# Optimization experiments

Measured on AMD Instinct MI355X. Metric: run time of the kernel, lower is better.

## Reference

```python
import jax, jax.numpy as jnp
import numpy as np

B, S, D, V = 256, 128, 768, 30522
MASK_ID = 103
# vocab ids of the label words (8 positive, 6 neutral, 7 negative)
LABEL_IDS = [
    [2307, 2204, 3835, 2157, 6581, 2986, 5151, 3893],
    [7929, 24791, 8699, 4257, 16021, 6623],
    [6659, 2919, 11771, 3532, 11325, 4997, 13135],
]


def setup_inputs() -> dict:
    key = jax.random.key(0)
    ks = jax.random.split(key, 12)
    length = jax.random.randint(ks[0], (B,), 5, 105)          # 3+length <= 108 < S
    input_ids = jax.random.randint(ks[1], (B, S), 200, 30000)  # never hits MASK_ID
    input_ids = input_ids.at[jnp.arange(B), 3 + length].set(MASK_ID)  # one [MASK] per row
    bert_out = jax.random.normal(ks[2], (B, S, D), dtype=jnp.float32)
    p = lambda k, shp: 0.02 * jax.random.normal(k, shp, dtype=jnp.float32)
    return {
        'bert_out': bert_out,
        'input_ids': input_ids,
        'length': length,
        'senti_w': p(ks[3], (2, D)), 'senti_b': p(ks[4], (2,)),
        'dense_w': p(ks[5], (D, 2 * D)), 'dense_b': p(ks[6], (D,)),
        'dec_w': p(ks[7], (V, D)), 'dec_b': p(ks[8], (V,)),
        'w0': p(ks[9], (2, 8)), 'w1': p(ks[10], (2, 6)), 'w2': p(ks[11], (2, 7)),
    }


def reference(bert_out, input_ids, length, senti_w, senti_b, dense_w, dense_b,
              dec_w, dec_b, w0, w1, w2):
    # pooler -> sentiment head (Dropout is identity at inference)
    pooler = bert_out[:, 0]                                   # [B, D]
    category_out = pooler @ senti_w.T + senti_b               # [B, 2]

    # per-row [MASK] hidden state (exactly one MASK_ID per row)
    mask_pos = jnp.argmax(input_ids == MASK_ID, axis=1)       # [B]
    mask_logits = jnp.take_along_axis(bert_out, mask_pos[:, None, None], axis=1)[:, 0]  # [B, D]

    # attention(): softmax over the ragged slice bert_out[i, 3:3+length[i]]
    scores_raw = jnp.einsum('bsd,bd->bs', bert_out, mask_logits)        # [B, S]
    idx = jnp.arange(S)
    valid = (idx[None, :] >= 3) & (idx[None, :] < 3 + length[:, None])  # [B, S]
    scores = jax.nn.softmax(jnp.where(valid, scores_raw, -jnp.inf), axis=1)
    scores = jnp.where(valid, scores, 0.0)
    att = jnp.einsum('bs,bsd->bd', scores, bert_out)          # [B, D]

    feats = jnp.concatenate([att, mask_logits], axis=1)       # [B, 2D]
    h = jnp.tanh(feats @ dense_w.T + dense_b)                 # [B, D]
    probs = jnp.tanh(h @ dec_w.T + dec_b)                     # [B, V]

    outs = []
    for ids, w in zip(LABEL_IDS, (w0, w1, w2)):
        lp = probs[:, jnp.array(ids)]                         # [B, k]
        outs.append(lp @ w.T)                                 # [B, 2]
    out = jnp.stack(outs, axis=2)                             # [B, 2, 3]
    return category_out, out
```

## Files before the change

### kernel.cpp

```cpp
#include <hip/hip_runtime.h>
#include <hip/hip_bf16.h>
#include <math.h>

#define BB 256
#define SS 128
#define DD 768
#define K2 1536
#define MASK_ID 103

typedef __attribute__((ext_vector_type(8))) short short8;
typedef __attribute__((ext_vector_type(4))) float floatx4;

__constant__ int c_ids[21] = {
    2307, 2204, 3835, 2157, 6581, 2986, 5151, 3893,
    7929, 24791, 8699, 4257, 16021, 6623,
    6659, 2919, 11771, 3532, 11325, 4997, 13135
};

__device__ __forceinline__ float waveReduceSum(float v) {
    #pragma unroll
    for (int off = 32; off > 0; off >>= 1) v += __shfl_down(v, off, 64);
    return v;
}
__device__ __forceinline__ float waveReduceSumAll(float v) {
    #pragma unroll
    for (int off = 32; off > 0; off >>= 1) v += __shfl_xor(v, off, 64);
    return v;
}
__device__ __forceinline__ unsigned short f2bf(float f) {
    unsigned int u = __float_as_uint(f);
    u += 0x7FFF + ((u >> 16) & 1);
    return (unsigned short)(u >> 16);
}

__global__ __launch_bounds__(256) void k_cvt(
    const float* __restrict__ src, unsigned short* __restrict__ dst, int n4)
{
    int i = blockIdx.x * 256 + threadIdx.x;
    if (i < n4) {
        float4 v = ((const float4*)src)[i];
        ushort4 o;
        o.x = f2bf(v.x); o.y = f2bf(v.y); o.z = f2bf(v.z); o.w = f2bf(v.w);
        ((ushort4*)dst)[i] = o;
    }
}

__global__ __launch_bounds__(1024) void k_att(
    const float* __restrict__ bert, const int* __restrict__ ids,
    const int* __restrict__ len, const float* __restrict__ senti_w,
    const float* __restrict__ senti_b, float* __restrict__ cat_out,
    unsigned short* __restrict__ feats)
{
    __shared__ __align__(16) float s_mask[DD];
    __shared__ __align__(16) float s_part[16][DD];
    __shared__ float s_m[16], s_l[16], s_scale[16];
    __shared__ float s_red[32];
    __shared__ float s_M;
    __shared__ int s_mp;

    const int b = blockIdx.x;
    const int tid = threadIdx.x;
    const int lane = tid & 63;
    const int wave = tid >> 6;

    if (tid == 0) s_mp = SS;
    __syncthreads();
    if (tid < SS && ids[b * SS + tid] == MASK_ID) atomicMin(&s_mp, tid);
    __syncthreads();
    const int mp = (s_mp == SS) ? 0 : s_mp;
    const int L = len[b];
    const float* base = bert + (size_t)b * SS * DD;
    const float* mrow = base + (size_t)mp * DD;

    float c0 = 0.f, c1 = 0.f;
    if (tid < DD) {
        s_mask[tid] = mrow[tid];
        float x = base[tid];
        c0 = x * senti_w[tid];
        c1 = x * senti_w[DD + tid];
    }
    c0 = waveReduceSum(c0);
    c1 = waveReduceSum(c1);
    if (lane == 0) { s_red[wave] = c0; s_red[16 + wave] = c1; }
    __syncthreads();
    if (tid == 0) {
        float t0 = 0.f, t1 = 0.f;
        #pragma unroll
        for (int w = 0; w < 16; ++w) { t0 += s_red[w]; t1 += s_red[16 + w]; }
        cat_out[b * 2 + 0] = t0 + senti_b[0];
        cat_out[b * 2 + 1] = t1 + senti_b[1];
    }

    const float4* m4 = (const float4*)s_mask;
    float4 mm0 = m4[lane], mm1 = m4[lane + 64], mm2 = m4[lane + 128];
    float4 A0 = {0,0,0,0}, A1 = {0,0,0,0}, A2 = {0,0,0,0};
    float mloc = -INFINITY, lloc = 0.f;
    for (int s = 3 + wave; s < 3 + L; s += 16) {
        const float4* row = (const float4*)(base + (size_t)s * DD);
        float4 r0 = row[lane], r1 = row[lane + 64], r2 = row[lane + 128];
        float d = r0.x * mm0.x + r0.y * mm0.y + r0.z * mm0.z + r0.w * mm0.w
                + r1.x * mm1.x + r1.y * mm1.y + r1.z * mm1.z + r1.w * mm1.w
                + r2.x * mm2.x + r2.y * mm2.y + r2.z * mm2.z + r2.w * mm2.w;
        d = waveReduceSumAll(d);
        float mnew = fmaxf(mloc, d);
        float scale = __expf(mloc - mnew);
        float p = __expf(d - mnew);
        lloc = lloc * scale + p;
        A0.x = A0.x * scale + p * r0.x; A0.y = A0.y * scale + p * r0.y;
        A0.z = A0.z * scale + p * r0.z; A0.w = A0.w * scale + p * r0.w;
        A1.x = A1.x * scale + p * r1.x; A1.y = A1.y * scale + p * r1.y;
        A1.z = A1.z * scale + p * r1.z; A1.w = A1.w * scale + p * r1.w;
        A2.x = A2.x * scale + p * r2.x; A2.y = A2.y * scale + p * r2.y;
        A2.z = A2.z * scale + p * r2.z; A2.w = A2.w * scale + p * r2.w;
        mloc = mnew;
    }
    if (lane == 0) { s_m[wave] = mloc; s_l[wave] = lloc; }
    float4* pw = (float4*)s_part[wave];
    pw[lane] = A0; pw[lane + 64] = A1; pw[lane + 128] = A2;
    __syncthreads();

    if (tid == 0) {
        float M = -INFINITY;
        #pragma unroll
        for (int w = 0; w < 16; ++w) M = fmaxf(M, s_m[w]);
        s_M = M;
    }
    __syncthreads();
    if (tid < 16) s_scale[tid] = __expf(s_m[tid] - s_M);
    __syncthreads();

    if (tid < DD) {
        float lt = 0.f, a = 0.f;
        #pragma unroll
        for (int w = 0; w < 16; ++w) {
            lt += s_scale[w] * s_l[w];
            a  += s_scale[w] * s_part[w][tid];
        }
        unsigned short* fb = feats + (size_t)b * K2;
        fb[tid]      = f2bf(a / lt);
        fb[DD + tid] = f2bf(s_mask[tid]);
    }
}

__global__ __launch_bounds__(256) void k_dense(
    const unsigned short* __restrict__ featsb,
    const unsigned short* __restrict__ dwb,
    const float* __restrict__ db, float* __restrict__ h)
{
    const int tid = threadIdx.x;
    const int lane = tid & 63, wave = tid >> 6;
    const int b0 = blockIdx.y * 32 + (wave >> 1) * 16;
    const int j0 = blockIdx.x * 32 + (wave & 1) * 16;
    const int m = lane & 15, q = lane >> 4;

    const short8* Arow = (const short8*)(featsb + (size_t)(b0 + m) * K2);
    const short8* Brow = (const short8*)(dwb + (size_t)(j0 + m) * K2);
    floatx4 acc = {0.f, 0.f, 0.f, 0.f};
    #pragma unroll 8
    for (int k8 = 0; k8 < K2 / 8; k8 += 4) {
        short8 a = Arow[k8 + q];
        short8 w = Brow[k8 + q];
        acc = __builtin_amdgcn_mfma_f32_16x16x32_bf16(a, w, acc, 0, 0, 0);
    }
    const int col = j0 + m;
    const int rb = b0 + q * 4;
    const float bias = db[col];
    #pragma unroll
    for (int r = 0; r < 4; ++r)
        h[(size_t)(rb + r) * DD + col] = tanhf(acc[r] + bias);
}

__global__ __launch_bounds__(256) void k_dec(
    const float* __restrict__ h, const float* __restrict__ dec_w,
    const float* __restrict__ dec_b, const float* __restrict__ w0,
    const float* __restrict__ w1, const float* __restrict__ w2,
    float* __restrict__ out)
{
    __shared__ __align__(16) float s_h[DD];
    __shared__ float s_p[21];
    const int b = blockIdx.x;
    const int tid = threadIdx.x;
    const int lane = tid & 63, wave = tid >> 6;

    for (int d = tid; d < DD; d += 256) s_h[d] = h[(size_t)b * DD + d];
    __syncthreads();

    for (int idx = wave; idx < 21; idx += 4) {
        const int vid = c_ids[idx];
        const float* wr = dec_w + (size_t)vid * DD;
        float acc = 0.f;
        #pragma unroll
        for (int i = 0; i < DD / 64; ++i)
            acc += s_h[lane + 64 * i] * wr[lane + 64 * i];
        acc = waveReduceSum(acc);
        if (lane == 0) s_p[idx] = tanhf(acc + dec_b[vid]);
    }
    __syncthreads();

    if (tid < 6) {
        const int c = tid / 3, g = tid % 3;
        const float* wg = (g == 0) ? w0 : (g == 1) ? w1 : w2;
        const int n    = (g == 0) ? 8  : (g == 1) ? 6  : 7;
        const int base = (g == 0) ? 0  : (g == 1) ? 8  : 14;
        float acc = 0.f;
        for (int i = 0; i < n; ++i) acc += s_p[base + i] * wg[c * n + i];
        out[(size_t)b * 6 + c * 3 + g] = acc;
    }
}

extern "C" void kernel_launch(void* const* d_in, const int* in_sizes, int n_in,
                              void* d_out, int out_size, void* d_ws, size_t ws_size,
                              hipStream_t stream) {
    const float* bert    = (const float*)d_in[0];
    const int*   ids     = (const int*)  d_in[1];
    const int*   len     = (const int*)  d_in[2];
    const float* senti_w = (const float*)d_in[3];
    const float* senti_b = (const float*)d_in[4];
    const float* dense_w = (const float*)d_in[5];
    const float* dense_b = (const float*)d_in[6];
    const float* dec_w   = (const float*)d_in[7];
    const float* dec_b   = (const float*)d_in[8];
    const float* w0      = (const float*)d_in[9];
    const float* w1      = (const float*)d_in[10];
    const float* w2      = (const float*)d_in[11];
    float* out = (float*)d_out;

    unsigned short* feats = (unsigned short*)d_ws;
    unsigned short* dwb   = feats + (size_t)BB * K2;
    float* h = (float*)(dwb + (size_t)DD * K2);

    const int n4 = DD * K2 / 4;
    k_cvt<<<(n4 + 255) / 256, 256, 0, stream>>>(dense_w, dwb, n4);
    k_att<<<BB, 1024, 0, stream>>>(bert, ids, len, senti_w, senti_b, out, feats);
    k_dense<<<dim3(24, 8), 256, 0, stream>>>(feats, dwb, dense_b, h);
    k_dec<<<BB, 256, 0, stream>>>(h, dec_w, dec_b, w0, w1, w2, out + BB * 2);
}
```

Measured before the change: 224.4 us.

## Fuse dense weight conversion into attention kernel, unroll rows, split-K dense GEMM

The separate fp32-to-bf16 conversion kernel for dense_w is removed and its work is spread across the attention kernel's blocks, saving one launch and overlapping the conversion with the attention reads. The online-softmax loop now processes two rows per wave per iteration to raise memory-level parallelism and halve the rescale steps. The dense MFMA kernel splits K across two wave groups with a shared-memory reduction, doubling the waves in flight for the small GEMM. The conversion adds memory traffic inside the attention kernel, and the split-K adds a block-level sync.

```diff
diff --git a/kernel.cpp b/kernel.cpp
--- a/kernel.cpp
+++ b/kernel.cpp
@@ -33,23 +33,12 @@
     return (unsigned short)(u >> 16);
 }
 
-__global__ __launch_bounds__(256) void k_cvt(
-    const float* __restrict__ src, unsigned short* __restrict__ dst, int n4)
-{
-    int i = blockIdx.x * 256 + threadIdx.x;
-    if (i < n4) {
-        float4 v = ((const float4*)src)[i];
-        ushort4 o;
-        o.x = f2bf(v.x); o.y = f2bf(v.y); o.z = f2bf(v.z); o.w = f2bf(v.w);
-        ((ushort4*)dst)[i] = o;
-    }
-}
-
 __global__ __launch_bounds__(1024) void k_att(
     const float* __restrict__ bert, const int* __restrict__ ids,
     const int* __restrict__ len, const float* __restrict__ senti_w,
     const float* __restrict__ senti_b, float* __restrict__ cat_out,
-    unsigned short* __restrict__ feats)
+    unsigned short* __restrict__ feats,
+    const float* __restrict__ dense_w, unsigned short* __restrict__ dwb)
 {
     __shared__ __align__(16) float s_mask[DD];
     __shared__ __align__(16) float s_part[16][DD];
@@ -64,6 +53,17 @@
     const int wave = tid >> 6;
 
     if (tid == 0) s_mp = SS;
+
+    {
+        const int n4 = DD * K2 / 4;
+        for (int i = b * 1024 + tid; i < n4; i += BB * 1024) {
+            float4 v = ((const float4*)dense_w)[i];
+            ushort4 o;
+            o.x = f2bf(v.x); o.y = f2bf(v.y); o.z = f2bf(v.z); o.w = f2bf(v.w);
+            ((ushort4*)dwb)[i] = o;
+        }
+    }
+
     __syncthreads();
     if (tid < SS && ids[b * SS + tid] == MASK_ID) atomicMin(&s_mp, tid);
     __syncthreads();
@@ -95,23 +95,50 @@
     float4 mm0 = m4[lane], mm1 = m4[lane + 64], mm2 = m4[lane + 128];
     float4 A0 = {0,0,0,0}, A1 = {0,0,0,0}, A2 = {0,0,0,0};
     float mloc = -INFINITY, lloc = 0.f;
-    for (int s = 3 + wave; s < 3 + L; s += 16) {
-        const float4* row = (const float4*)(base + (size_t)s * DD);
-        float4 r0 = row[lane], r1 = row[lane + 64], r2 = row[lane + 128];
-        float d = r0.x * mm0.x + r0.y * mm0.y + r0.z * mm0.z + r0.w * mm0.w
-                + r1.x * mm1.x + r1.y * mm1.y + r1.z * mm1.z + r1.w * mm1.w
-                + r2.x * mm2.x + r2.y * mm2.y + r2.z * mm2.z + r2.w * mm2.w;
-        d = waveReduceSumAll(d);
-        float mnew = fmaxf(mloc, d);
+    int s = 3 + wave;
+    for (; s + 16 < 3 + L; s += 32) {
+        const float4* ra = (const float4*)(base + (size_t)s * DD);
+        const float4* rb = (const float4*)(base + (size_t)(s + 16) * DD);
+        float4 a0 = ra[lane], a1 = ra[lane + 64], a2 = ra[lane + 128];
+        float4 b0 = rb[lane], b1 = rb[lane + 64], b2 = rb[lane + 128];
+        float d1 = a0.x*mm0.x + a0.y*mm0.y + a0.z*mm0.z + a0.w*mm0.w
+                 + a1.x*mm1.x + a1.y*mm1.y + a1.z*mm1.z + a1.w*mm1.w
+                 + a2.x*mm2.x + a2.y*mm2.y + a2.z*mm2.z + a2.w*mm2.w;
+        float d2 = b0.x*mm0.x + b0.y*mm0.y + b0.z*mm0.z + b0.w*mm0.w
+                 + b1.x*mm1.x + b1.y*mm1.y + b1.z*mm1.z + b1.w*mm1.w
+                 + b2.x*mm2.x + b2.y*mm2.y + b2.z*mm2.z + b2.w*mm2.w;
+        d1 = waveReduceSumAll(d1);
+        d2 = waveReduceSumAll(d2);
+        float mnew = fmaxf(mloc, fmaxf(d1, d2));
         float scale = __expf(mloc - mnew);
-        float p = __expf(d - mnew);
-        lloc = lloc * scale + p;
-        A0.x = A0.x * scale + p * r0.x; A0.y = A0.y * scale + p * r0.y;
-        A0.z = A0.z * scale + p * r0.z; A0.w = A0.w * scale + p * r0.w;
-        A1.x = A1.x * scale + p * r1.x; A1.y = A1.y * scale + p * r1.y;
-        A1.z = A1.z * scale + p * r1.z; A1.w = A1.w * scale + p * r1.w;
-        A2.x = A2.x * scale + p * r2.x; A2.y = A2.y * scale + p * r2.y;
-        A2.z = A2.z * scale + p * r2.z; A2.w = A2.w * scale + p * r2.w;
+        float p1 = __expf(d1 - mnew);
+        float p2 = __expf(d2 - mnew);
+        lloc = lloc * scale + p1 + p2;
+        A0.x = A0.x*scale + p1*a0.x + p2*b0.x; A0.y = A0.y*scale + p1*a0.y + p2*b0.y;
+        A0.z = A0.z*scale + p1*a0.z + p2*b0.z; A0.w = A0.w*scale + p1*a0.w + p2*b0.w;
+        A1.x = A1.x*scale + p1*a1.x + p2*b1.x; A1.y = A1.y*scale + p1*a1.y + p2*b1.y;
+        A1.z = A1.z*scale + p1*a1.z + p2*b1.z; A1.w = A1.w*scale + p1*a1.w + p2*b1.w;
+        A2.x = A2.x*scale + p1*a2.x + p2*b2.x; A2.y = A2.y*scale + p1*a2.y + p2*b2.y;
+        A2.z = A2.z*scale + p1*a2.z + p2*b2.z; A2.w = A2.w*scale + p1*a2.w + p2*b2.w;
+        mloc = mnew;
+    }
+    for (; s < 3 + L; s += 16) {
+        const float4* ra = (const float4*)(base + (size_t)s * DD);
+        float4 a0 = ra[lane], a1 = ra[lane + 64], a2 = ra[lane + 128];
+        float d1 = a0.x*mm0.x + a0.y*mm0.y + a0.z*mm0.z + a0.w*mm0.w
+                 + a1.x*mm1.x + a1.y*mm1.y + a1.z*mm1.z + a1.w*mm1.w
+                 + a2.x*mm2.x + a2.y*mm2.y + a2.z*mm2.z + a2.w*mm2.w;
+        d1 = waveReduceSumAll(d1);
+        float mnew = fmaxf(mloc, d1);
+        float scale = __expf(mloc - mnew);
+        float p1 = __expf(d1 - mnew);
+        lloc = lloc * scale + p1;
+        A0.x = A0.x*scale + p1*a0.x; A0.y = A0.y*scale + p1*a0.y;
+        A0.z = A0.z*scale + p1*a0.z; A0.w = A0.w*scale + p1*a0.w;
+        A1.x = A1.x*scale + p1*a1.x; A1.y = A1.y*scale + p1*a1.y;
+        A1.z = A1.z*scale + p1*a1.z; A1.w = A1.w*scale + p1*a1.w;
+        A2.x = A2.x*scale + p1*a2.x; A2.y = A2.y*scale + p1*a2.y;
+        A2.z = A2.z*scale + p1*a2.z; A2.w = A2.w*scale + p1*a2.w;
         mloc = mnew;
     }
     if (lane == 0) { s_m[wave] = mloc; s_l[wave] = lloc; }
@@ -142,32 +169,40 @@
     }
 }
 
-__global__ __launch_bounds__(256) void k_dense(
+__global__ __launch_bounds__(512) void k_dense(
     const unsigned short* __restrict__ featsb,
     const unsigned short* __restrict__ dwb,
     const float* __restrict__ db, float* __restrict__ h)
 {
+    __shared__ floatx4 s_acc[4][64];
     const int tid = threadIdx.x;
     const int lane = tid & 63, wave = tid >> 6;
-    const int b0 = blockIdx.y * 32 + (wave >> 1) * 16;
-    const int j0 = blockIdx.x * 32 + (wave & 1) * 16;
+    const int wq = wave & 3, kh = wave >> 2;
+    const int b0 = blockIdx.y * 32 + (wq >> 1) * 16;
+    const int j0 = blockIdx.x * 32 + (wq & 1) * 16;
     const int m = lane & 15, q = lane >> 4;
 
-    const short8* Arow = (const short8*)(featsb + (size_t)(b0 + m) * K2);
-    const short8* Brow = (const short8*)(dwb + (size_t)(j0 + m) * K2);
+    const short8* Arow = (const short8*)(featsb + (size_t)(b0 + m) * K2) + kh * 96;
+    const short8* Brow = (const short8*)(dwb + (size_t)(j0 + m) * K2) + kh * 96;
     floatx4 acc = {0.f, 0.f, 0.f, 0.f};
-    #pragma unroll 8
-    for (int k8 = 0; k8 < K2 / 8; k8 += 4) {
+    #pragma unroll 6
+    for (int k8 = 0; k8 < 96; k8 += 4) {
         short8 a = Arow[k8 + q];
         short8 w = Brow[k8 + q];
         acc = __builtin_amdgcn_mfma_f32_16x16x32_bf16(a, w, acc, 0, 0, 0);
     }
-    const int col = j0 + m;
-    const int rb = b0 + q * 4;
-    const float bias = db[col];
-    #pragma unroll
-    for (int r = 0; r < 4; ++r)
-        h[(size_t)(rb + r) * DD + col] = tanhf(acc[r] + bias);
+    if (kh) s_acc[wq][lane] = acc;
+    __syncthreads();
+    if (!kh) {
+        floatx4 o = s_acc[wq][lane];
+        acc.x += o.x; acc.y += o.y; acc.z += o.z; acc.w += o.w;
+        const int col = j0 + m;
+        const int rb = b0 + q * 4;
+        const float bias = db[col];
+        #pragma unroll
+        for (int r = 0; r < 4; ++r)
+            h[(size_t)(rb + r) * DD + col] = tanhf(acc[r] + bias);
+    }
 }
 
 __global__ __launch_bounds__(256) void k_dec(
@@ -229,9 +264,8 @@
     unsigned short* dwb   = feats + (size_t)BB * K2;
     float* h = (float*)(dwb + (size_t)DD * K2);
 
-    const int n4 = DD * K2 / 4;
-    k_cvt<<<(n4 + 255) / 256, 256, 0, stream>>>(dense_w, dwb, n4);
-    k_att<<<BB, 1024, 0, stream>>>(bert, ids, len, senti_w, senti_b, out, feats);
-    k_dense<<<dim3(24, 8), 256, 0, stream>>>(feats, dwb, dense_b, h);
+    k_att<<<BB, 1024, 0, stream>>>(bert, ids, len, senti_w, senti_b, out,
+                                   feats, dense_w, dwb);
+    k_dense<<<dim3(24, 8), 512, 0, stream>>>(feats, dwb, dense_b, h);
     k_dec<<<BB, 256, 0, stream>>>(h, dec_w, dec_b, w0, w1, w2, out + BB * 2);
 }
```

Measured after the change: 222.4 us. Within noise of the previous version (-0.9%).
